# Kernel tuning notes

Hardware: AMD Instinct MI355X
Metric: run time of the kernel (lower is better)

The kernel has to match this reference:

```python
import jax, jax.numpy as jnp
import numpy as np

KERNEL = 3
STRIDE = 1
PADDING = 1


def _extract_patches(x, k, stride, padding, h_out, w_out):
    # x: [B, C, H, W] -> patches [k, k, B, C, h_out, w_out]
    if padding > 0:
        x = jnp.pad(x, ((0, 0), (0, 0), (padding, padding), (padding, padding)))
    rows = []
    for di in range(k):
        cols = []
        for dj in range(k):
            sl = x[:, :, di:di + (h_out - 1) * stride + 1:stride,
                        dj:dj + (w_out - 1) * stride + 1:stride]
            cols.append(sl)
        rows.append(jnp.stack(cols, axis=0))
    return jnp.stack(rows, axis=0)  # [k, k, B, C, h_out, w_out]


def setup_inputs() -> dict:
    key = jax.random.key(0)
    k1, k2 = jax.random.split(key)
    B, C_in, C_out, H, W = 32, 64, 64, 32, 32
    h_out = (H + 2 * PADDING - KERNEL) // STRIDE + 1
    w_out = (W + 2 * PADDING - KERNEL) // STRIDE + 1
    fan_in = C_in * KERNEL ** 2
    x = jax.random.normal(k1, (B, C_in, H, W), dtype=jnp.float32)
    weight = jax.random.normal(
        k2, (h_out, w_out, C_out, C_in, KERNEL, KERNEL), dtype=jnp.float32
    ) / np.sqrt(fan_in).astype(np.float32)
    bias = jnp.zeros((C_out, h_out, w_out), dtype=jnp.float32)
    return {"x": x, "weight": weight, "bias": bias}


def reference(x, weight, bias):
    h_out, w_out = weight.shape[0], weight.shape[1]
    # patches: [k, k, B, C, h_out, w_out]
    patches = _extract_patches(x, KERNEL, STRIDE, PADDING, h_out, w_out)
    # unshared-weight contraction per spatial location
    # weight: [h_out(x), w_out(y), O, C(i), k(k), k(l)]
    out = jnp.einsum('xyoikl,klbixy->boxy', weight, patches)
    return out + bias[None, :, :, :]
```

## Files before the change

### kernel.cpp

```cpp
#include <hip/hip_runtime.h>

#define HH 32
#define WW 32
#define CIN 64
#define COUT 64
#define BATCH 32
#define KTOT 576
#define NPOS 1024
#define KC 16
#define KHALF 288
#define NCW 18
#define WGRP 260

__device__ float g_xT[CIN * 34 * 34 * BATCH];

__global__ __launch_bounds__(256) void repack_kernel(const float* __restrict__ x) {
    __shared__ float tile[32 * 33];
    const int i   = blockIdx.x;
    const int hh  = blockIdx.y;
    const int tid = threadIdx.x;

    float* dst = &g_xT[((i * 34 + hh) * 34) * BATCH];

    if (hh == 0 || hh == 33) {
        for (int idx = tid; idx < 34 * BATCH; idx += 256) dst[idx] = 0.f;
        return;
    }
    const int hs = hh - 1;
#pragma unroll
    for (int bb = 0; bb < 4; ++bb) {
        int b = bb * 8 + (tid >> 5);
        int w = tid & 31;
        tile[b * 33 + w] = x[(b << 16) + (i << 10) + (hs << 5) + w];
    }
    __syncthreads();
#pragma unroll
    for (int q = 0; q < 5; ++q) {
        int ww = q * 8 + (tid >> 5);
        if (ww < 34) {
            int b = tid & 31;
            float v = (ww == 0 || ww == 33) ? 0.f : tile[b * 33 + (ww - 1)];
            dst[ww * BATCH + b] = v;
        }
    }
}

__device__ __forceinline__ void async16(const void* src, void* dst_lds) {
    __builtin_amdgcn_global_load_lds(
        (const __attribute__((address_space(1))) void*)src,
        (__attribute__((address_space(3))) void*)dst_lds,
        16, 0, 0);
}

__global__ __launch_bounds__(128, 2) void local2d_kernel(
    const float* __restrict__ weight,
    const float* __restrict__ bias,
    float* __restrict__ out)
{
    __shared__ float Wl[2][3][4 * WGRP];
    __shared__ float Pl[2][3][KC * BATCH];

    const int wv = threadIdx.x >> 6;
    const int l  = threadIdx.x & 63;

    const int og = l & 7, bg = l >> 3;

    int bid = blockIdx.x;
    int xcd = bid & 7;
    int t   = bid >> 3;
    int y   = ((t >> 5) << 3) | xcd;
    int xw  = t & 31;
    int p   = (y << 5) | xw;

    const int kbase = wv * KHALF;
    const float* wpos  = weight + (long)p * (COUT * KTOT);
    const float* wsrc0 = wpos + (l >> 2) * KTOT + ((l & 3) << 2) + kbase;

    float acc[8][4];
#pragma unroll
    for (int a = 0; a < 8; ++a)
#pragma unroll
        for (int c = 0; c < 4; ++c) acc[a][c] = 0.f;

    auto stage = [&](int c, int bsel) {
        const float* ws = wsrc0 + c * KC;
#pragma unroll
        for (int g = 0; g < 4; ++g)
            async16(ws + g * (16 * KTOT), &Wl[wv][bsel][g * WGRP]);
#pragma unroll
        for (int q = 0; q < 2; ++q) {
            int k  = kbase + c * KC + (q << 3) + (l >> 3);
            int i  = k / 9;
            int r  = k - i * 9;
            int kh = r / 3;
            int kw = r - kh * 3;
            const float* ps =
                &g_xT[(((i * 34) + y + kh) * 34 + xw + kw) * BATCH + ((l & 7) << 2)];
            async16(ps, &Pl[wv][bsel][q * (8 * BATCH)]);
        }
    };

    auto compute = [&](int bsel) {
        const float* Wb = &Wl[wv][bsel][(og >> 1) * WGRP + ((og & 1) << 3) * 16];
        const float* Pb = &Pl[wv][bsel][bg << 2];
#pragma unroll
        for (int kk = 0; kk < KC; kk += 4) {
            float4 pr[4];
#pragma unroll
            for (int j = 0; j < 4; ++j)
                pr[j] = *(const float4*)(Pb + (kk + j) * BATCH);
            const float* prf = (const float*)pr;
#pragma unroll
            for (int oo = 0; oo < 8; ++oo) {
                float4 wr = *(const float4*)(Wb + oo * KC + kk);
#pragma unroll
                for (int bb = 0; bb < 4; ++bb) {
                    float a = acc[oo][bb];
                    a = fmaf(wr.x, prf[0 * 4 + bb], a);
                    a = fmaf(wr.y, prf[1 * 4 + bb], a);
                    a = fmaf(wr.z, prf[2 * 4 + bb], a);
                    a = fmaf(wr.w, prf[3 * 4 + bb], a);
                    acc[oo][bb] = a;
                }
            }
        }
    };

    stage(0, 0);
    stage(1, 1);
    for (int c = 0; c < NCW - 1; ++c) {
        asm volatile("s_waitcnt vmcnt(6)" ::: "memory");
        asm volatile("s_waitcnt lgkmcnt(0)" ::: "memory");
        if (c + 2 < NCW) stage(c + 2, (c + 2) % 3);
        compute(c % 3);
    }
    asm volatile("s_waitcnt vmcnt(0)" ::: "memory");
    compute((NCW - 1) % 3);

    __syncthreads();
    float* R = &Wl[1][0][0];
    if (wv == 1) {
#pragma unroll
        for (int oo = 0; oo < 8; ++oo) {
            int o = (og << 3) + oo;
            *(float4*)(&R[o * 36 + (bg << 2)]) =
                make_float4(acc[oo][0], acc[oo][1], acc[oo][2], acc[oo][3]);
        }
    }
    __syncthreads();
    if (wv == 0) {
#pragma unroll
        for (int oo = 0; oo < 8; ++oo) {
            int o = (og << 3) + oo;
            float bv = bias[(o << 10) + p];
            float4 r = *(const float4*)(&R[o * 36 + (bg << 2)]);
            const float* rf = (const float*)&r;
#pragma unroll
            for (int bb = 0; bb < 4; ++bb) {
                int b = (bg << 2) + bb;
                out[(b << 16) + (o << 10) + p] = acc[oo][bb] + rf[bb] + bv;
            }
        }
    }
}

extern "C" void kernel_launch(void* const* d_in, const int* in_sizes, int n_in,
                              void* d_out, int out_size, void* d_ws, size_t ws_size,
                              hipStream_t stream) {
    const float* x      = (const float*)d_in[0];
    const float* weight = (const float*)d_in[1];
    const float* bias   = (const float*)d_in[2];
    float* out          = (float*)d_out;

    hipLaunchKernelGGL(repack_kernel, dim3(CIN, 34), dim3(256), 0, stream, x);
    hipLaunchKernelGGL(local2d_kernel, dim3(NPOS), dim3(128), 0, stream,
                       weight, bias, out);
}
```

Baseline: 239.3 us.

## Replace FP32 FMA GEMM with bf16 MFMA using register-direct loads

The per-position 64x576 by 576x32 contraction moves off scalar FP32 FMAs onto bf16 16x16x32 MFMA instructions. Weights and patches are converted to bf16 in registers on the fly. The LDS async staging is replaced by direct global-to-register loads (nontemporal for weights) with a three-deep register buffer, and the k-split reduction through LDS is dropped. Each wave now owns 32 output channels across the full K. This targets compute cost, but the kernel is likely bound by streaming the weight tensor, and bf16 rounding over K=576 adds error that may exceed tolerance.

```diff
diff --git a/kernel.cpp b/kernel.cpp
--- a/kernel.cpp
+++ b/kernel.cpp
@@ -1,16 +1,12 @@
 #include <hip/hip_runtime.h>
+#include <hip/hip_bf16.h>
 
-#define HH 32
-#define WW 32
 #define CIN 64
 #define COUT 64
 #define BATCH 32
 #define KTOT 576
 #define NPOS 1024
-#define KC 16
-#define KHALF 288
-#define NCW 18
-#define WGRP 260
+#define NKS 18
 
 __device__ float g_xT[CIN * 34 * 34 * BATCH];
 
@@ -45,11 +41,14 @@
     }
 }
 
-__device__ __forceinline__ void async16(const void* src, void* dst_lds) {
-    __builtin_amdgcn_global_load_lds(
-        (const __attribute__((address_space(1))) void*)src,
-        (__attribute__((address_space(3))) void*)dst_lds,
-        16, 0, 0);
+typedef __attribute__((ext_vector_type(8))) short bf16x8;
+typedef __attribute__((ext_vector_type(4))) float f32x4;
+typedef __attribute__((ext_vector_type(4))) float f32x4v;
+
+union Frag { bf16x8 v; __hip_bfloat162 h[4]; };
+
+__device__ __forceinline__ __hip_bfloat162 cvt2(float a, float b) {
+    return __float22bfloat162_rn(make_float2(a, b));
 }
 
 __global__ __launch_bounds__(128, 2) void local2d_kernel(
@@ -57,13 +56,10 @@
     const float* __restrict__ bias,
     float* __restrict__ out)
 {
-    __shared__ float Wl[2][3][4 * WGRP];
-    __shared__ float Pl[2][3][KC * BATCH];
-
     const int wv = threadIdx.x >> 6;
     const int l  = threadIdx.x & 63;
-
-    const int og = l & 7, bg = l >> 3;
+    const int lm = l & 15;
+    const int a4 = l >> 4;
 
     int bid = blockIdx.x;
     int xcd = bid & 7;
@@ -72,94 +68,81 @@
     int xw  = t & 31;
     int p   = (y << 5) | xw;
 
-    const int kbase = wv * KHALF;
-    const float* wpos  = weight + (long)p * (COUT * KTOT);
-    const float* wsrc0 = wpos + (l >> 2) * KTOT + ((l & 3) << 2) + kbase;
+    const float* w0 = weight + ((long)p * COUT + (wv * 32 + lm)) * KTOT + a4 * 8;
+    const float* w1 = w0 + 16 * KTOT;
 
-    float acc[8][4];
+    const float* pbase = g_xT + ((y * 34) + xw) * BATCH + lm;
+
+    f32x4 acc[2][2];
 #pragma unroll
-    for (int a = 0; a < 8; ++a)
+    for (int i0 = 0; i0 < 2; ++i0)
 #pragma unroll
-        for (int c = 0; c < 4; ++c) acc[a][c] = 0.f;
+        for (int i1 = 0; i1 < 2; ++i1) acc[i0][i1] = (f32x4){0.f, 0.f, 0.f, 0.f};
 
-    auto stage = [&](int c, int bsel) {
-        const float* ws = wsrc0 + c * KC;
+    f32x4v wbuf[3][2][2];
+    float  pbuf[3][2][8];
+
+    auto issue = [&](int ks, int d) {
+        wbuf[d][0][0] = __builtin_nontemporal_load((const f32x4v*)(w0 + ks * 32));
+        wbuf[d][0][1] = __builtin_nontemporal_load((const f32x4v*)(w0 + ks * 32 + 4));
+        wbuf[d][1][0] = __builtin_nontemporal_load((const f32x4v*)(w1 + ks * 32));
+        wbuf[d][1][1] = __builtin_nontemporal_load((const f32x4v*)(w1 + ks * 32 + 4));
 #pragma unroll
-        for (int g = 0; g < 4; ++g)
-            async16(ws + g * (16 * KTOT), &Wl[wv][bsel][g * WGRP]);
-#pragma unroll
-        for (int q = 0; q < 2; ++q) {
-            int k  = kbase + c * KC + (q << 3) + (l >> 3);
-            int i  = k / 9;
-            int r  = k - i * 9;
-            int kh = r / 3;
-            int kw = r - kh * 3;
-            const float* ps =
-                &g_xT[(((i * 34) + y + kh) * 34 + xw + kw) * BATCH + ((l & 7) << 2)];
-            async16(ps, &Pl[wv][bsel][q * (8 * BATCH)]);
+        for (int j = 0; j < 8; ++j) {
+            int k  = ks * 32 + a4 * 8 + j;
+            int i  = (k * 7282) >> 16;
+            int r  = k - 9 * i;
+            int kh = (r * 11) >> 5;
+            int kw = r - 3 * kh;
+            const float* rp = pbase + (i * 1156 + kh * 34 + kw) * BATCH;
+            pbuf[d][0][j] = rp[0];
+            pbuf[d][1][j] = rp[16];
         }
     };
 
-    auto compute = [&](int bsel) {
-        const float* Wb = &Wl[wv][bsel][(og >> 1) * WGRP + ((og & 1) << 3) * 16];
-        const float* Pb = &Pl[wv][bsel][bg << 2];
+    auto consume = [&](int d) {
+        Frag A[2], B[2];
 #pragma unroll
-        for (int kk = 0; kk < KC; kk += 4) {
-            float4 pr[4];
+        for (int t2 = 0; t2 < 2; ++t2) {
+            A[t2].h[0] = cvt2(wbuf[d][t2][0].x, wbuf[d][t2][0].y);
+            A[t2].h[1] = cvt2(wbuf[d][t2][0].z, wbuf[d][t2][0].w);
+            A[t2].h[2] = cvt2(wbuf[d][t2][1].x, wbuf[d][t2][1].y);
+            A[t2].h[3] = cvt2(wbuf[d][t2][1].z, wbuf[d][t2][1].w);
+            B[t2].h[0] = cvt2(pbuf[d][t2][0], pbuf[d][t2][1]);
+            B[t2].h[1] = cvt2(pbuf[d][t2][2], pbuf[d][t2][3]);
+            B[t2].h[2] = cvt2(pbuf[d][t2][4], pbuf[d][t2][5]);
+            B[t2].h[3] = cvt2(pbuf[d][t2][6], pbuf[d][t2][7]);
+        }
 #pragma unroll
-            for (int j = 0; j < 4; ++j)
-                pr[j] = *(const float4*)(Pb + (kk + j) * BATCH);
-            const float* prf = (const float*)pr;
+        for (int t2 = 0; t2 < 2; ++t2)
 #pragma unroll
-            for (int oo = 0; oo < 8; ++oo) {
-                float4 wr = *(const float4*)(Wb + oo * KC + kk);
-#pragma unroll
-                for (int bb = 0; bb < 4; ++bb) {
-                    float a = acc[oo][bb];
-                    a = fmaf(wr.x, prf[0 * 4 + bb], a);
-                    a = fmaf(wr.y, prf[1 * 4 + bb], a);
-                    a = fmaf(wr.z, prf[2 * 4 + bb], a);
-                    a = fmaf(wr.w, prf[3 * 4 + bb], a);
-                    acc[oo][bb] = a;
-                }
-            }
-        }
+            for (int bt = 0; bt < 2; ++bt)
+                acc[t2][bt] = __builtin_amdgcn_mfma_f32_16x16x32_bf16(
+                    A[t2].v, B[bt].v, acc[t2][bt], 0, 0, 0);
     };
 
-    stage(0, 0);
-    stage(1, 1);
-    for (int c = 0; c < NCW - 1; ++c) {
-        asm volatile("s_waitcnt vmcnt(6)" ::: "memory");
-        asm volatile("s_waitcnt lgkmcnt(0)" ::: "memory");
-        if (c + 2 < NCW) stage(c + 2, (c + 2) % 3);
-        compute(c % 3);
+    issue(0, 0);
+    issue(1, 1);
+#pragma unroll
+    for (int ks = 0; ks < NKS; ++ks) {
+        if (ks + 2 < NKS) issue(ks + 2, (ks + 2) % 3);
+        consume(ks % 3);
     }
-    asm volatile("s_waitcnt vmcnt(0)" ::: "memory");
-    compute((NCW - 1) % 3);
 
-    __syncthreads();
-    float* R = &Wl[1][0][0];
-    if (wv == 1) {
 #pragma unroll
-        for (int oo = 0; oo < 8; ++oo) {
-            int o = (og << 3) + oo;
-            *(float4*)(&R[o * 36 + (bg << 2)]) =
-                make_float4(acc[oo][0], acc[oo][1], acc[oo][2], acc[oo][3]);
-        }
-    }
-    __syncthreads();
-    if (wv == 0) {
+    for (int t2 = 0; t2 < 2; ++t2) {
+        int obase = wv * 32 + t2 * 16 + a4 * 4;
+        float bv[4];
 #pragma unroll
-        for (int oo = 0; oo < 8; ++oo) {
-            int o = (og << 3) + oo;
-            float bv = bias[(o << 10) + p];
-            float4 r = *(const float4*)(&R[o * 36 + (bg << 2)]);
-            const float* rf = (const float*)&r;
+        for (int reg = 0; reg < 4; ++reg)
+            bv[reg] = bias[((obase + reg) << 10) + p];
 #pragma unroll
-            for (int bb = 0; bb < 4; ++bb) {
-                int b = (bg << 2) + bb;
-                out[(b << 16) + (o << 10) + p] = acc[oo][bb] + rf[bb] + bv;
-            }
+        for (int bt = 0; bt < 2; ++bt) {
+            int b = bt * 16 + lm;
+#pragma unroll
+            for (int reg = 0; reg < 4; ++reg)
+                out[(b << 16) + ((obase + reg) << 10) + p] =
+                    acc[t2][bt][reg] + bv[reg];
         }
     }
 }
```

New measurement: 245.2 us. 2.4% more time.
